# Kernel tuning notes

Measured on AMD Instinct MI355X. Metric: run time of the kernel, lower is better.

## Reference

```python
import jax, jax.numpy as jnp
import numpy as np

B, N, DIM, H = 64, 196, 1024, 32
HD = DIM // H  # 32, must equal H for the bias broadcast quirk
S = 14  # sqrt(num_patches)


def _relative_position_index(s):
    coords = np.stack(np.meshgrid(np.arange(s), np.arange(s), indexing='ij'))  # [2,s,s]
    cf = coords.reshape(2, -1)  # [2, N]
    rel = (cf[:, :, None] - cf[:, None, :]).transpose(1, 2, 0)  # [N,N,2]
    rel[..., 0] += s - 1
    rel[..., 1] += s - 1
    rel[..., 0] *= 2 * s - 1
    return rel.sum(-1).astype(np.int32)  # [N,N], values in [0, (2s-1)^2)


def setup_inputs() -> dict:
    key = jax.random.key(0)
    k0, k1, k2, k3 = jax.random.split(key, 4)
    x = jax.random.normal(k0, (B, N, DIM), dtype=jnp.float32)
    W_qkv = jax.random.normal(k1, (DIM, 3 * DIM), dtype=jnp.float32) * 0.02
    W_proj = jax.random.normal(k2, (DIM, DIM), dtype=jnp.float32) * 0.02
    b_proj = jnp.zeros((DIM,), dtype=jnp.float32)
    rpk = jax.random.normal(k3, ((2 * S - 1) ** 2, HD), dtype=jnp.float32)  # [729, HD]
    rel_idx = jnp.asarray(_relative_position_index(S))  # [N, N] int32
    return {"x": x, "W_qkv": W_qkv, "W_proj": W_proj, "b_proj": b_proj,
            "rpk": rpk, "rel_idx": rel_idx}


def reference(x, W_qkv, W_proj, b_proj, rpk, rel_idx):
    b, n, c = x.shape
    scale = HD ** -0.5
    qkv = (x @ W_qkv).reshape(b, n, 3, H, HD)  # [B,N,3,H,HD]
    q, k, v = jnp.moveaxis(qkv, 2, 0)          # each [B,N,H,HD]
    q = q.transpose(0, 2, 1, 3)                # [B,H,N,HD]
    k = k.transpose(0, 2, 1, 3)
    v = v.transpose(0, 2, 1, 3)
    attn = jnp.einsum('bhnd,bhmd->bhnm', q, k) * scale  # [B,H,N,N]
    # gather relative-position bias: [N*N, HD] -> [N,N,HD] -> [HD,N,N]
    bias = rpk[rel_idx.reshape(-1)].reshape(n, n, HD).transpose(2, 0, 1)
    attn = jax.nn.softmax(attn + bias[None], axis=-1)   # bias broadcasts since HD == H
    out = jnp.einsum('bhnm,bhmd->bhnd', attn, v)        # [B,H,N,HD]
    out = out.transpose(0, 2, 1, 3).reshape(b, n, c)    # [B,N,C]
    return out @ W_proj + b_proj
```

## Files before the change

### kernel.cpp

```cpp
#include <hip/hip_runtime.h>
#include <hip/hip_bf16.h>

typedef __bf16 bf16_t;
typedef __attribute__((ext_vector_type(8))) __bf16 bf16x8;
typedef __attribute__((ext_vector_type(4))) __bf16 bf16x4;
typedef __attribute__((ext_vector_type(4))) float f32x4;

#define NPOS 38416
#define NPAD 224
#define KSTR 40
#define VSTR 232

__device__ __forceinline__ void async_copy16(const bf16_t* g, bf16_t* l) {
  __builtin_amdgcn_global_load_lds((const __attribute__((address_space(1))) void*)g,
                                   (__attribute__((address_space(3))) void*)l, 16, 0, 0);
}

__global__ __launch_bounds__(256) void cast_x_kernel(const float* __restrict__ x,
                                                     bf16_t* __restrict__ xb, int n4) {
  int i = blockIdx.x * 256 + threadIdx.x;
  if (i < n4) {
    float4 v = ((const float4*)x)[i];
    bf16x4 o;
    o[0] = (bf16_t)v.x; o[1] = (bf16_t)v.y; o[2] = (bf16_t)v.z; o[3] = (bf16_t)v.w;
    ((bf16x4*)xb)[i] = o;
  }
}

__global__ __launch_bounds__(256) void transpose_cast_kernel(const float* __restrict__ src,
                                                             bf16_t* __restrict__ dst,
                                                             int K, int Ncols) {
  __shared__ float tile[32][33];
  int t = threadIdx.x;
  int tx = t & 31, ty = t >> 5;
  int bx = blockIdx.x, by = blockIdx.y;
  for (int r = ty; r < 32; r += 8)
    tile[r][tx] = src[(size_t)(by * 32 + r) * Ncols + bx * 32 + tx];
  __syncthreads();
  for (int r = ty; r < 32; r += 8)
    dst[(size_t)(bx * 32 + r) * K + by * 32 + tx] = (bf16_t)tile[tx][r];
}

__global__ __launch_bounds__(256) void bias_gather_kernel(const float* __restrict__ rpk,
                                                          const int* __restrict__ rel_idx,
                                                          float* __restrict__ bias) {
  int pos = blockIdx.x * 256 + threadIdx.x;
  if (pos < NPOS) {
    int idx = rel_idx[pos];
    const float* r = rpk + idx * 32;
#pragma unroll
    for (int h = 0; h < 32; ++h) bias[h * NPOS + pos] = r[h];
  }
}

template <int MODE>
__global__ __launch_bounds__(512, 4) void gemm_bt_kernel(
    const bf16_t* __restrict__ A, const bf16_t* __restrict__ Bt,
    bf16_t* __restrict__ qo, bf16_t* __restrict__ ko, bf16_t* __restrict__ vto,
    float* __restrict__ fo, const float* __restrict__ bp) {
  constexpr int K = 1024;
  constexpr int CH = 384 * 32;
  __shared__ alignas(16) bf16_t S[2][CH];
  const int t = threadIdx.x;
  const int lane = t & 63;
  const int quad = lane >> 4;
  const int l16 = lane & 15;
  const int wave = t >> 6;

  const int GX = gridDim.x;
  const int nwg = GX * gridDim.y;
  const int lin = blockIdx.y * GX + blockIdx.x;
  const int qch = nwg >> 3, rch = nwg & 7;
  const int xcd = lin & 7, off = lin >> 3;
  const int swz = (xcd < rch ? xcd * (qch + 1) : rch * (qch + 1) + (xcd - rch) * qch) + off;
  const int m0 = (swz / GX) * 256, n0 = (swz % GX) * 128;

  const int wr = (wave >> 1) * 64, wc = (wave & 1) * 64;

  const bf16_t* gp[3];
  int lofs[3];
#pragma unroll
  for (int j = 0; j < 3; ++j) {
    const int c = t + j * 512;
    const int row = c >> 2;
    const int sc = (c & 3) ^ ((c >> 3) & 3);
    gp[j] = (row < 256) ? A + (size_t)(m0 + row) * K + sc * 8
                        : Bt + (size_t)(n0 + row - 256) * K + sc * 8;
    lofs[j] = c * 8;
  }

  const int qa = quad ^ ((l16 >> 1) & 3);

  const f32x4 vzero = {0.f, 0.f, 0.f, 0.f};
  f32x4 acc[4][4];
#pragma unroll
  for (int i = 0; i < 4; ++i)
#pragma unroll
    for (int j = 0; j < 4; ++j) acc[i][j] = vzero;

#pragma unroll
  for (int j = 0; j < 3; ++j) async_copy16(gp[j], &S[0][lofs[j]]);

  for (int it = 0; it < K / 32; ++it) {
    __syncthreads();
    const bf16_t* Sb = S[it & 1];
    if (it + 1 < K / 32) {
      bf16_t* Sn = S[(it + 1) & 1];
      const int kt = (it + 1) * 32;
#pragma unroll
      for (int j = 0; j < 3; ++j) async_copy16(gp[j] + kt, Sn + lofs[j]);
    }
    const bf16_t* As = Sb;
    const bf16_t* Bs = Sb + 256 * 32;
    bf16x8 af[4], bfr[4];
#pragma unroll
    for (int i = 0; i < 4; ++i) {
      af[i] = *(const bf16x8*)(As + (wr + i * 16 + l16) * 32 + qa * 8);
      bfr[i] = *(const bf16x8*)(Bs + (wc + i * 16 + l16) * 32 + qa * 8);
    }
#pragma unroll
    for (int i = 0; i < 4; ++i)
#pragma unroll
      for (int j = 0; j < 4; ++j)
        acc[i][j] = __builtin_amdgcn_mfma_f32_16x16x32_bf16(af[i], bfr[j], acc[i][j], 0, 0, 0);
  }

  if (MODE == 0) {
    const float qscale = 0.17677669529663687f;
    const int which = n0 >> 10;
#pragma unroll
    for (int i = 0; i < 4; ++i) {
      const int rb = m0 + wr + i * 16 + quad * 4;
#pragma unroll
      for (int j = 0; j < 4; ++j) {
        const int c = n0 + wc + j * 16 + l16;
        const int h = (c >> 5) & 31, d = c & 31;
#pragma unroll
        for (int r = 0; r < 4; ++r) {
          const int rg = rb + r;
          const int b = rg / 196, n = rg - b * 196;
          const float v = acc[i][j][r];
          if (which == 0)
            qo[(((size_t)b * 32 + h) * 196 + n) * 32 + d] = (bf16_t)(v * qscale);
          else if (which == 1)
            ko[(((size_t)b * 32 + h) * 196 + n) * 32 + d] = (bf16_t)v;
          else
            vto[(((size_t)b * 32 + h) * 32 + d) * 196 + n] = (bf16_t)v;
        }
      }
    }
  } else {
#pragma unroll
    for (int i = 0; i < 4; ++i) {
      const int rb = m0 + wr + i * 16 + quad * 4;
#pragma unroll
      for (int j = 0; j < 4; ++j) {
        const int c = n0 + wc + j * 16 + l16;
        const float bias_c = bp[c];
#pragma unroll
        for (int r = 0; r < 4; ++r)
          fo[(size_t)(rb + r) * 1024 + c] = acc[i][j][r] + bias_c;
      }
    }
  }
}

__global__ __launch_bounds__(256, 2) void attn_kernel(
    const bf16_t* __restrict__ q, const bf16_t* __restrict__ kmat,
    const bf16_t* __restrict__ vtg, const float* __restrict__ bias,
    bf16_t* __restrict__ attn_out) {
  __shared__ alignas(16) bf16_t kf[NPAD * KSTR];
  __shared__ alignas(16) bf16_t vts[32 * VSTR];
  __shared__ alignas(16) bf16_t pb[4][16 * VSTR];

  const int t = threadIdx.x;
  const int lane = t & 63;
  const int quad = lane >> 4, l16 = lane & 15;
  const int wave = t >> 6;
  const int bh = blockIdx.x;
  const int b = bh >> 5, h = bh & 31;
  const bf16_t* qg = q + (size_t)bh * (196 * 32);
  const bf16_t* kg = kmat + (size_t)bh * (196 * 32);
  const bf16_t* vg = vtg + (size_t)bh * (32 * 196);
  const float* bg = bias + (size_t)h * NPOS;

  {
    const uint4* src = (const uint4*)kg;
    uint4* dst = (uint4*)kf;
    for (int c = t; c < 784; c += 256) dst[(c >> 2) * 5 + (c & 3)] = src[c];
    const uint4 z4 = {0u, 0u, 0u, 0u};
    if (t < 112) {
      int r = 196 + (t >> 2), ch = t & 3;
      dst[r * 5 + ch] = z4;
    }
    const uint2 z2 = {0u, 0u};
    for (int i = t; i < 1792; i += 256) {
      int d = i / 56, c = i - d * 56;
      uint2 val = (c < 49) ? ((const uint2*)(vg + d * 196))[c] : z2;
      ((uint2*)(vts + d * VSTR))[c] = val;
    }
  }
  __syncthreads();

  const f32x4 vzero = {0.f, 0.f, 0.f, 0.f};
  bf16_t* pw = &pb[wave][0];

  for (int ch = wave; ch < 13; ch += 4) {
    const int q0 = ch * 16;
    int qrow = q0 + l16;
    if (qrow > 195) qrow = 195;
    const bf16x8 aq = *(const bf16x8*)(qg + qrow * 32 + quad * 8);

    float bv[13][4];
#pragma unroll
    for (int ct = 0; ct < 13; ++ct) {
      const int col = ct * 16 + l16;
#pragma unroll
      for (int r = 0; r < 4; ++r) {
        int br = q0 + quad * 4 + r;
        if (br > 195) br = 195;
        bv[ct][r] = (col < 196) ? bg[br * 196 + col] : 0.f;
      }
    }

    f32x4 s[13];
#pragma unroll
    for (int ct = 0; ct < 13; ++ct) {
      const bf16x8 bk = *(const bf16x8*)(kf + (ct * 16 + l16) * KSTR + quad * 8);
      s[ct] = __builtin_amdgcn_mfma_f32_16x16x32_bf16(aq, bk, vzero, 0, 0, 0);
    }
#pragma unroll
    for (int ct = 0; ct < 13; ++ct) {
      const int col = ct * 16 + l16;
#pragma unroll
      for (int r = 0; r < 4; ++r) {
        if (col < 196)
          s[ct][r] += bv[ct][r];
        else
          s[ct][r] = -1e30f;
      }
    }
    float mx[4], inv[4];
#pragma unroll
    for (int r = 0; r < 4; ++r) {
      float m = s[0][r];
#pragma unroll
      for (int ct = 1; ct < 13; ++ct) m = fmaxf(m, s[ct][r]);
      m = fmaxf(m, __shfl_xor(m, 1));
      m = fmaxf(m, __shfl_xor(m, 2));
      m = fmaxf(m, __shfl_xor(m, 4));
      m = fmaxf(m, __shfl_xor(m, 8));
      mx[r] = m;
    }
#pragma unroll
    for (int ct = 0; ct < 13; ++ct)
#pragma unroll
      for (int r = 0; r < 4; ++r) s[ct][r] = __expf(s[ct][r] - mx[r]);
#pragma unroll
    for (int r = 0; r < 4; ++r) {
      float sum = s[0][r];
#pragma unroll
      for (int ct = 1; ct < 13; ++ct) sum += s[ct][r];
      sum += __shfl_xor(sum, 1);
      sum += __shfl_xor(sum, 2);
      sum += __shfl_xor(sum, 4);
      sum += __shfl_xor(sum, 8);
      inv[r] = 1.f / sum;
    }
#pragma unroll
    for (int ct = 0; ct < 13; ++ct) {
      const int col = ct * 16 + l16;
#pragma unroll
      for (int r = 0; r < 4; ++r) pw[(quad * 4 + r) * VSTR + col] = (bf16_t)s[ct][r];
    }
    if (lane < 32) {
      const bf16x8 z8 = {};
      *(bf16x8*)(pw + (lane >> 1) * VSTR + 208 + (lane & 1) * 8) = z8;
    }
#pragma unroll
    for (int dt = 0; dt < 2; ++dt) {
      f32x4 o = vzero;
#pragma unroll
      for (int kk = 0; kk < 7; ++kk) {
        const bf16x8 ap = *(const bf16x8*)(pw + l16 * VSTR + kk * 32 + quad * 8);
        const bf16x8 bv2 = *(const bf16x8*)(vts + (dt * 16 + l16) * VSTR + kk * 32 + quad * 8);
        o = __builtin_amdgcn_mfma_f32_16x16x32_bf16(ap, bv2, o, 0, 0, 0);
      }
      const int d = dt * 16 + l16;
#pragma unroll
      for (int r = 0; r < 4; ++r) {
        const int n = q0 + quad * 4 + r;
        if (n < 196)
          attn_out[(((size_t)b * 196 + n) * 32 + h) * 32 + d] = (bf16_t)(o[r] * inv[r]);
      }
    }
  }
}

extern "C" void kernel_launch(void* const* d_in, const int* in_sizes, int n_in,
                              void* d_out, int out_size, void* d_ws, size_t ws_size,
                              hipStream_t stream) {
  (void)in_sizes; (void)n_in; (void)out_size; (void)ws_size;
  const float* x = (const float*)d_in[0];
  const float* Wqkv = (const float*)d_in[1];
  const float* Wproj = (const float*)d_in[2];
  const float* bproj = (const float*)d_in[3];
  const float* rpk = (const float*)d_in[4];
  const int* rel_idx = (const int*)d_in[5];
  float* out = (float*)d_out;

  char* ws = (char*)d_ws;
  bf16_t* xb = (bf16_t*)(ws + 0);
  bf16_t* wqkvT = (bf16_t*)(ws + 25690112);
  bf16_t* wprojT = (bf16_t*)(ws + 31981568);
  bf16_t* q = (bf16_t*)(ws + 34078720);
  bf16_t* kk = (bf16_t*)(ws + 59768832);
  bf16_t* vt = (bf16_t*)(ws + 85458944);
  float* bias = (float*)(ws + 111149056);
  bf16_t* attn = xb;

  cast_x_kernel<<<12544, 256, 0, stream>>>(x, xb, 12845056 / 4);
  transpose_cast_kernel<<<dim3(96, 32), 256, 0, stream>>>(Wqkv, wqkvT, 1024, 3072);
  transpose_cast_kernel<<<dim3(32, 32), 256, 0, stream>>>(Wproj, wprojT, 1024, 1024);
  bias_gather_kernel<<<151, 256, 0, stream>>>(rpk, rel_idx, bias);
  gemm_bt_kernel<0><<<dim3(24, 49), 512, 0, stream>>>(xb, wqkvT, q, kk, vt, nullptr, nullptr);
  attn_kernel<<<2048, 256, 0, stream>>>(q, kk, vt, bias, attn);
  gemm_bt_kernel<1><<<dim3(8, 49), 512, 0, stream>>>(attn, wprojT, nullptr, nullptr, nullptr, out, bproj);
}
```

Baseline: 342.9 us.

## Software-pipeline bias loads across attention chunks with double-buffered registers

Unrolls the per-wave chunk loop into explicit iterations and double-buffers the gathered bias values in registers. The next chunk's bias is fetched from global memory while the current chunk's PV MFMAs run, and the first chunk's bias load is issued before the K/V shared-memory staging. It also adds s_setprio around the MFMA blocks and tree-shaped max/sum reductions. Holding two 52-float bias buffers raises register pressure under the 2-blocks-per-CU launch bound and could cause spills.

```diff
diff --git a/kernel.cpp b/kernel.cpp
--- a/kernel.cpp
+++ b/kernel.cpp
@@ -165,6 +165,92 @@
   }
 }
 
+#define LOADB(Q0, BV)                                                         \
+  _Pragma("unroll") for (int ct = 0; ct < 13; ++ct) {                         \
+    const int col = ct * 16 + l16;                                            \
+    _Pragma("unroll") for (int r = 0; r < 4; ++r) {                           \
+      int br = (Q0) + quad * 4 + r;                                           \
+      if (br > 195) br = 195;                                                 \
+      BV[ct][r] = (col < 196) ? bg[br * 196 + col] : 0.f;                     \
+    }                                                                         \
+  }
+
+#define AITER(Q0, BVC, QN, BVN, PREF)                                         \
+  {                                                                           \
+    const int q0_ = (Q0);                                                     \
+    int qrow_ = q0_ + l16;                                                    \
+    if (qrow_ > 195) qrow_ = 195;                                             \
+    const bf16x8 aq_ = *(const bf16x8*)(qg + qrow_ * 32 + quad * 8);          \
+    f32x4 s[13];                                                              \
+    __builtin_amdgcn_s_setprio(1);                                            \
+    _Pragma("unroll") for (int ct = 0; ct < 13; ++ct) {                       \
+      const bf16x8 bk_ = *(const bf16x8*)(kf + (ct * 16 + l16) * KSTR + quad * 8); \
+      s[ct] = __builtin_amdgcn_mfma_f32_16x16x32_bf16(aq_, bk_, vzero, 0, 0, 0); \
+    }                                                                         \
+    __builtin_amdgcn_s_setprio(0);                                            \
+    _Pragma("unroll") for (int ct = 0; ct < 13; ++ct) {                       \
+      const int col = ct * 16 + l16;                                          \
+      _Pragma("unroll") for (int r = 0; r < 4; ++r) {                         \
+        if (col < 196) s[ct][r] += BVC[ct][r];                                \
+        else s[ct][r] = -1e30f;                                               \
+      }                                                                       \
+    }                                                                         \
+    float mx[4], inv[4];                                                      \
+    _Pragma("unroll") for (int r = 0; r < 4; ++r) {                           \
+      float p0_ = fmaxf(s[0][r], s[1][r]), p1_ = fmaxf(s[2][r], s[3][r]);     \
+      float p2_ = fmaxf(s[4][r], s[5][r]), p3_ = fmaxf(s[6][r], s[7][r]);     \
+      float p4_ = fmaxf(s[8][r], s[9][r]), p5_ = fmaxf(s[10][r], s[11][r]);   \
+      float m_ = fmaxf(fmaxf(fmaxf(p0_, p1_), fmaxf(p2_, p3_)),               \
+                       fmaxf(fmaxf(p4_, p5_), s[12][r]));                     \
+      m_ = fmaxf(m_, __shfl_xor(m_, 1));                                      \
+      m_ = fmaxf(m_, __shfl_xor(m_, 2));                                      \
+      m_ = fmaxf(m_, __shfl_xor(m_, 4));                                      \
+      m_ = fmaxf(m_, __shfl_xor(m_, 8));                                      \
+      mx[r] = m_;                                                             \
+    }                                                                         \
+    _Pragma("unroll") for (int ct = 0; ct < 13; ++ct)                         \
+      _Pragma("unroll") for (int r = 0; r < 4; ++r)                           \
+        s[ct][r] = __expf(s[ct][r] - mx[r]);                                  \
+    _Pragma("unroll") for (int r = 0; r < 4; ++r) {                           \
+      float a0_ = (s[0][r] + s[1][r]) + (s[2][r] + s[3][r]);                  \
+      float a1_ = (s[4][r] + s[5][r]) + (s[6][r] + s[7][r]);                  \
+      float a2_ = (s[8][r] + s[9][r]) + (s[10][r] + s[11][r]);                \
+      float sum_ = a0_ + a1_ + (a2_ + s[12][r]);                              \
+      sum_ += __shfl_xor(sum_, 1);                                            \
+      sum_ += __shfl_xor(sum_, 2);                                            \
+      sum_ += __shfl_xor(sum_, 4);                                            \
+      sum_ += __shfl_xor(sum_, 8);                                            \
+      inv[r] = 1.f / sum_;                                                    \
+    }                                                                         \
+    _Pragma("unroll") for (int ct = 0; ct < 13; ++ct) {                       \
+      const int col = ct * 16 + l16;                                          \
+      _Pragma("unroll") for (int r = 0; r < 4; ++r)                           \
+        pw[(quad * 4 + r) * VSTR + col] = (bf16_t)s[ct][r];                   \
+    }                                                                         \
+    if (lane < 32) {                                                          \
+      const bf16x8 z8_ = {};                                                  \
+      *(bf16x8*)(pw + (lane >> 1) * VSTR + 208 + (lane & 1) * 8) = z8_;       \
+    }                                                                         \
+    if (PREF) { LOADB((QN), BVN); }                                           \
+    _Pragma("unroll") for (int dt = 0; dt < 2; ++dt) {                        \
+      f32x4 o_ = vzero;                                                       \
+      __builtin_amdgcn_s_setprio(1);                                          \
+      _Pragma("unroll") for (int kk2 = 0; kk2 < 7; ++kk2) {                   \
+        const bf16x8 ap_ = *(const bf16x8*)(pw + l16 * VSTR + kk2 * 32 + quad * 8); \
+        const bf16x8 bv2_ = *(const bf16x8*)(vts + (dt * 16 + l16) * VSTR + kk2 * 32 + quad * 8); \
+        o_ = __builtin_amdgcn_mfma_f32_16x16x32_bf16(ap_, bv2_, o_, 0, 0, 0); \
+      }                                                                       \
+      __builtin_amdgcn_s_setprio(0);                                          \
+      const int d_ = dt * 16 + l16;                                           \
+      _Pragma("unroll") for (int r = 0; r < 4; ++r) {                         \
+        const int n_ = q0_ + quad * 4 + r;                                    \
+        if (n_ < 196)                                                         \
+          attn_out[(((size_t)b * 196 + n_) * 32 + h) * 32 + d_] =             \
+              (bf16_t)(o_[r] * inv[r]);                                       \
+      }                                                                       \
+    }                                                                         \
+  }
+
 __global__ __launch_bounds__(256, 2) void attn_kernel(
     const bf16_t* __restrict__ q, const bf16_t* __restrict__ kmat,
     const bf16_t* __restrict__ vtg, const float* __restrict__ bias,
@@ -184,6 +270,9 @@
   const bf16_t* vg = vtg + (size_t)bh * (32 * 196);
   const float* bg = bias + (size_t)h * NPOS;
 
+  float bvA[13][4], bvB[13][4];
+  LOADB(wave * 16, bvA);
+
   {
     const uint4* src = (const uint4*)kg;
     uint4* dst = (uint4*)kf;
@@ -205,96 +294,11 @@
   const f32x4 vzero = {0.f, 0.f, 0.f, 0.f};
   bf16_t* pw = &pb[wave][0];
 
-  for (int ch = wave; ch < 13; ch += 4) {
-    const int q0 = ch * 16;
-    int qrow = q0 + l16;
-    if (qrow > 195) qrow = 195;
-    const bf16x8 aq = *(const bf16x8*)(qg + qrow * 32 + quad * 8);
-
-    float bv[13][4];
-#pragma unroll
-    for (int ct = 0; ct < 13; ++ct) {
-      const int col = ct * 16 + l16;
-#pragma unroll
-      for (int r = 0; r < 4; ++r) {
-        int br = q0 + quad * 4 + r;
-        if (br > 195) br = 195;
-        bv[ct][r] = (col < 196) ? bg[br * 196 + col] : 0.f;
-      }
-    }
-
-    f32x4 s[13];
-#pragma unroll
-    for (int ct = 0; ct < 13; ++ct) {
-      const bf16x8 bk = *(const bf16x8*)(kf + (ct * 16 + l16) * KSTR + quad * 8);
-      s[ct] = __builtin_amdgcn_mfma_f32_16x16x32_bf16(aq, bk, vzero, 0, 0, 0);
-    }
-#pragma unroll
-    for (int ct = 0; ct < 13; ++ct) {
-      const int col = ct * 16 + l16;
-#pragma unroll
-      for (int r = 0; r < 4; ++r) {
-        if (col < 196)
-          s[ct][r] += bv[ct][r];
-        else
-          s[ct][r] = -1e30f;
-      }
-    }
-    float mx[4], inv[4];
-#pragma unroll
-    for (int r = 0; r < 4; ++r) {
-      float m = s[0][r];
-#pragma unroll
-      for (int ct = 1; ct < 13; ++ct) m = fmaxf(m, s[ct][r]);
-      m = fmaxf(m, __shfl_xor(m, 1));
-      m = fmaxf(m, __shfl_xor(m, 2));
-      m = fmaxf(m, __shfl_xor(m, 4));
-      m = fmaxf(m, __shfl_xor(m, 8));
-      mx[r] = m;
-    }
-#pragma unroll
-    for (int ct = 0; ct < 13; ++ct)
-#pragma unroll
-      for (int r = 0; r < 4; ++r) s[ct][r] = __expf(s[ct][r] - mx[r]);
-#pragma unroll
-    for (int r = 0; r < 4; ++r) {
-      float sum = s[0][r];
-#pragma unroll
-      for (int ct = 1; ct < 13; ++ct) sum += s[ct][r];
-      sum += __shfl_xor(sum, 1);
-      sum += __shfl_xor(sum, 2);
-      sum += __shfl_xor(sum, 4);
-      sum += __shfl_xor(sum, 8);
-      inv[r] = 1.f / sum;
-    }
-#pragma unroll
-    for (int ct = 0; ct < 13; ++ct) {
-      const int col = ct * 16 + l16;
-#pragma unroll
-      for (int r = 0; r < 4; ++r) pw[(quad * 4 + r) * VSTR + col] = (bf16_t)s[ct][r];
-    }
-    if (lane < 32) {
-      const bf16x8 z8 = {};
-      *(bf16x8*)(pw + (lane >> 1) * VSTR + 208 + (lane & 1) * 8) = z8;
-    }
-#pragma unroll
-    for (int dt = 0; dt < 2; ++dt) {
-      f32x4 o = vzero;
-#pragma unroll
-      for (int kk = 0; kk < 7; ++kk) {
-        const bf16x8 ap = *(const bf16x8*)(pw + l16 * VSTR + kk * 32 + quad * 8);
-        const bf16x8 bv2 = *(const bf16x8*)(vts + (dt * 16 + l16) * VSTR + kk * 32 + quad * 8);
-        o = __builtin_amdgcn_mfma_f32_16x16x32_bf16(ap, bv2, o, 0, 0, 0);
-      }
-      const int d = dt * 16 + l16;
-#pragma unroll
-      for (int r = 0; r < 4; ++r) {
-        const int n = q0 + quad * 4 + r;
-        if (n < 196)
-          attn_out[(((size_t)b * 196 + n) * 32 + h) * 32 + d] = (bf16_t)(o[r] * inv[r]);
-      }
-    }
-  }
+  AITER(wave * 16, bvA, (wave + 4) * 16, bvB, true);
+  AITER((wave + 4) * 16, bvB, (wave + 8) * 16, bvA, true);
+  AITER((wave + 8) * 16, bvA, (wave + 12) * 16, bvB, (wave + 12 < 13));
+  if (wave + 12 < 13)
+    AITER((wave + 12) * 16, bvB, 0, bvA, false);
 }
 
 extern "C" void kernel_launch(void* const* d_in, const int* in_sizes, int n_in,
```

Result: no change. 341.8 us (-0.3%).
